# Performance work log

Measured on AMD Instinct MI355X. Metric: run time of the kernel, lower is better.

Reference implementation:

```python
import jax, jax.numpy as jnp
import numpy as np
from jax import lax

B, C_IN, H_IN, W_IN = 128, 256, 8, 32
RH, RW = 16, 64            # rec-head resolution
YOH, XOH = RH // 2, RW // 2  # onehot sizes (8, 32)
HID = 256
NC = 163                   # num classes == embed size
T = 32                     # target length
C_ENC = C_IN + XOH + YOH   # 296 encoder channels
L = (RH // 2) * (RW // 2)  # 256 attention positions


def setup_inputs() -> dict:
    key = jax.random.key(0)
    ks = jax.random.split(key, 18)
    s = 0.05
    return {
        "x": jax.random.normal(ks[0], (B, C_IN, H_IN, W_IN), jnp.float32),
        "decoder_targets": jax.random.randint(ks[1], (B, T), 0, NC),
        "word_targets": jax.random.randint(ks[2], (B, T), 0, NC),
        # seq_encoder conv 3x3
        "conv_w": jax.random.normal(ks[3], (C_IN, C_IN, 3, 3), jnp.float32) * 0.02,
        "conv_b": jnp.zeros((C_IN,), jnp.float32),
        # decoder embedding (post kaiming re-init => random, not identity)
        "emb_dec": jax.random.normal(ks[4], (NC, NC), jnp.float32) * s,
        "word_w": jax.random.normal(ks[5], (HID, NC), jnp.float32) * s,
        "word_b": jnp.zeros((HID,), jnp.float32),
        "attn_w": jax.random.normal(ks[6], (HID, 2 * HID + XOH + YOH), jnp.float32) * s,
        "attn_b": jnp.zeros((HID,), jnp.float32),
        "attn_v": jax.random.normal(ks[7], (HID,), jnp.float32) * (1.0 / np.sqrt(HID)),
        # GRUCell, gate order [r, z, n]
        "gru_wih": jax.random.normal(ks[8], (3 * HID, 2 * HID + XOH + YOH), jnp.float32) * s,
        "gru_bih": jnp.zeros((3 * HID,), jnp.float32),
        "gru_whh": jax.random.normal(ks[9], (3 * HID, HID), jnp.float32) * s,
        "gru_bhh": jnp.zeros((3 * HID,), jnp.float32),
        "out_w": jax.random.normal(ks[10], (NC, HID), jnp.float32) * s,
        "out_b": jnp.zeros((NC,), jnp.float32),
        # positional one-hot embedding tables (also kaiming re-initialized)
        "x_emb": jax.random.normal(ks[11], (XOH, XOH), jnp.float32) * s,
        "y_emb": jax.random.normal(ks[12], (YOH, YOH), jnp.float32) * s,
    }


def _forward(x, conv_w, conv_b, emb_dec, word_w, word_b, attn_w, attn_b, attn_v,
             gru_wih, gru_bih, gru_whh, gru_bhh, out_w, out_b, x_emb, y_emb,
             decoder_targets, word_targets):
    b = x.shape[0]
    # rescale: bilinear upsample (align_corners=False ~ half-pixel)
    xr = jax.image.resize(x, (b, C_IN, RH, RW), method="linear")
    # seq_encoder: conv3x3 + ReLU + maxpool2
    conv = lax.conv_general_dilated(xr, conv_w, (1, 1), "SAME",
                                    dimension_numbers=("NCHW", "OIHW", "NCHW"))
    conv = jax.nn.relu(conv + conv_b[None, :, None, None])
    pooled = lax.reduce_window(conv, -jnp.inf, lax.max,
                               (1, 1, 2, 2), (1, 1, 2, 2), "VALID")  # (B,256,8,32)
    hf, wf = RH // 2, RW // 2
    # positional channels: x_map[c,y,x] = x_emb[x,c]; y_map[c,y,x] = y_emb[y,c]
    x_map = jnp.broadcast_to(x_emb.T[:, None, :], (XOH, hf, wf))
    y_map = jnp.broadcast_to(y_emb.T[:, :, None], (YOH, hf, wf))
    x_map = jnp.broadcast_to(x_map[None], (b, XOH, hf, wf))
    y_map = jnp.broadcast_to(y_map[None], (b, YOH, hf, wf))
    feat = jnp.concatenate([pooled, x_map, y_map], axis=1)      # (B,296,8,32)
    enc = feat.reshape(b, C_ENC, hf * wf).transpose(0, 2, 1)    # (B, L, C)

    t_len = decoder_targets.shape[1]
    # teacher forcing: input at step 0 is BOS (=0), else previous target
    inputs_seq = jnp.concatenate(
        [jnp.zeros((b, 1), decoder_targets.dtype), decoder_targets[:, :-1]], axis=1)

    def step(hidden, xs):
        tok, tgt = xs
        we = emb_dec[tok] @ word_w.T + word_b                   # (B, HID)
        # Bahdanau attention
        hrep = jnp.broadcast_to(hidden[:, None, :], (b, enc.shape[1], HID))
        cat = jnp.concatenate([hrep, enc], axis=-1)             # (B,L,2H+OH)
        energy = jnp.tanh(jnp.einsum("blc,hc->blh", cat, attn_w) + attn_b)
        scores = jnp.einsum("blh,h->bl", energy, attn_v)
        w = jax.nn.softmax(scores, axis=1)                      # (B,L)
        ctx = jnp.einsum("bl,blc->bc", w, enc)                  # (B, C)
        rin = jnp.concatenate([we, ctx], axis=-1)               # (B, 2H+OH)
        # GRUCell
        gi = rin @ gru_wih.T + gru_bih
        gh = hidden @ gru_whh.T + gru_bhh
        i_r, i_z, i_n = jnp.split(gi, 3, axis=-1)
        h_r, h_z, h_n = jnp.split(gh, 3, axis=-1)
        r = jax.nn.sigmoid(i_r + h_r)
        z = jax.nn.sigmoid(i_z + h_z)
        n = jnp.tanh(i_n + r * h_n)
        h_new = (1.0 - z) * n + z * hidden
        logp = jax.nn.log_softmax(h_new @ out_w.T + out_b, axis=1)
        # NLLLoss(ignore_index=-1, reduction='none')
        nll = -jnp.take_along_axis(logp, jnp.clip(tgt, 0)[:, None], axis=1)[:, 0]
        nll = jnp.where(tgt >= 0, nll, 0.0)
        return h_new, nll

    h0 = jnp.zeros((b, HID), jnp.float32)
    _, nlls = lax.scan(step, h0, (inputs_seq.T, word_targets.T))  # (T, B)
    loss_vec = nlls.sum(axis=0)                                   # (B,)
    return 0.2 * (loss_vec.sum() / loss_vec.shape[0])


def reference(x, decoder_targets, word_targets, conv_w, conv_b, emb_dec,
              word_w, word_b, attn_w, attn_b, attn_v, gru_wih, gru_bih,
              gru_whh, gru_bhh, out_w, out_b, x_emb, y_emb):
    return _forward(x, conv_w, conv_b, emb_dec, word_w, word_b, attn_w, attn_b,
                    attn_v, gru_wih, gru_bih, gru_whh, gru_bhh, out_w, out_b,
                    x_emb, y_emb, decoder_targets, word_targets)
```

## Files before the change

### kernel.cpp

```cpp
#include <hip/hip_runtime.h>
#include <hip/hip_bf16.h>
#include <math.h>

#define B    128
#define CIN  256
#define HIN  8
#define WIN_ 32
#define RH   16
#define RW   64
#define HID  256
#define NC   163
#define T    32
#define L    256
#define CENC 296

typedef __attribute__((ext_vector_type(8))) short short8;
typedef __attribute__((ext_vector_type(8))) unsigned short u16x8;
typedef __attribute__((ext_vector_type(4))) float f32x4;

#define PH(k) ((((k) >> 3) * 12) + ((k) & 7))

__device__ __forceinline__ float bf2f(unsigned short u) {
    unsigned int x = ((unsigned int)u) << 16;
    return __uint_as_float(x);
}
__device__ __forceinline__ unsigned short f2bf(float f) {
    unsigned int x = __float_as_uint(f);
    unsigned int r = (x + 0x7FFFu + ((x >> 16) & 1u)) >> 16;
    return (unsigned short)r;
}
__device__ __forceinline__ float fast_tanh(float x) {
    float e = __expf(2.f * x);
    return 1.f - 2.f * __builtin_amdgcn_rcpf(e + 1.f);
}
__device__ __forceinline__ float fast_sigm(float x) {
    return __builtin_amdgcn_rcpf(1.f + __expf(-x));
}
__device__ __forceinline__ float wave_red_max(float v) {
    #pragma unroll
    for (int o = 32; o > 0; o >>= 1) v = fmaxf(v, __shfl_down(v, o, 64));
    return v;
}
__device__ __forceinline__ float wave_red_sum(float v) {
    #pragma unroll
    for (int o = 32; o > 0; o >>= 1) v += __shfl_down(v, o, 64);
    return v;
}
__device__ __forceinline__ float half_red_sum(float v) {
    #pragma unroll
    for (int o = 16; o > 0; o >>= 1) v += __shfl_down(v, o, 64);
    return v;
}

__global__ void __launch_bounds__(256) k_upsxt(const float* __restrict__ x,
                                               unsigned short* __restrict__ Xt) {
    __shared__ __align__(16) float sf[64 * 2 * 32];
    const int y = blockIdx.x;
    const int b = blockIdx.y;
    const int tid = threadIdx.x;
    float sy = 0.5f * y - 0.25f;
    int yq0 = (y - 1) >> 1;
    float wy = sy - (float)yq0;
    int y0c = min(max(yq0, 0), HIN - 1);
    int y1c = min(max(yq0 + 1, 0), HIN - 1);
    const int xo = tid & 63;
    const int cj = tid >> 6;
    float sx = 0.5f * xo - 0.25f;
    int xq0 = (xo - 1) >> 1;
    float wx = sx - (float)xq0;
    int x0c = min(max(xq0, 0), WIN_ - 1);
    int x1c = min(max(xq0 + 1, 0), WIN_ - 1);
    for (int cc = 0; cc < 4; cc++) {
        __syncthreads();
        #pragma unroll
        for (int i = 0; i < 4; i++) {
            int idx = tid * 4 + i;
            int c = idx >> 4;
            int rowh = (idx >> 3) & 1;
            int part = idx & 7;
            int ysrc = rowh ? y1c : y0c;
            float4 v = *reinterpret_cast<const float4*>(
                x + ((size_t)(b * CIN + cc * 64 + c) * HIN + ysrc) * WIN_ + part * 4);
            *reinterpret_cast<float4*>(sf + ((c * 2 + rowh) * 32 + part * 4)) = v;
        }
        __syncthreads();
        unsigned short ov[16];
        #pragma unroll
        for (int j = 0; j < 16; j++) {
            int c = cj * 16 + j;
            const float* r0 = sf + (c * 2 + 0) * 32;
            const float* r1 = sf + (c * 2 + 1) * 32;
            float v = (1.f - wy) * ((1.f - wx) * r0[x0c] + wx * r0[x1c])
                    +        wy  * ((1.f - wx) * r1[x0c] + wx * r1[x1c]);
            ov[j] = f2bf(v);
        }
        unsigned short* dst = Xt + ((size_t)((b * 16 + y) * 64 + xo)) * 256 + cc * 64 + cj * 16;
        *reinterpret_cast<u16x8*>(dst)     = *reinterpret_cast<u16x8*>(ov);
        *reinterpret_cast<u16x8*>(dst + 8) = *reinterpret_cast<u16x8*>(ov + 8);
    }
}

__global__ void k_wt(const float* __restrict__ conv_w, unsigned short* __restrict__ Wt) {
    int e = blockIdx.x * 256 + threadIdx.x;
    int ci = e & 255;
    int co = (e >> 8) & 255;
    int s  = e >> 16;
    Wt[(size_t)(s * 256 + co) * 256 + ci] = f2bf(conv_w[(size_t)(co * 256 + ci) * 9 + s]);
}

__global__ void __launch_bounds__(256) k_convmm(const unsigned short* __restrict__ Xt,
        const unsigned short* __restrict__ Wt, const float* __restrict__ conv_b,
        unsigned short* __restrict__ enc_bf) {
    __shared__ __align__(16) char smem[34048];
    unsigned short* A_s = (unsigned short*)smem;
    unsigned short* B_s = A_s + 128 * 40;
    float* pool = (float*)smem;
    const int mt = blockIdx.x;
    const int n0 = blockIdx.y * 128;
    const int b = mt >> 3;
    const int y0 = (mt & 7) * 2;
    const int tid = threadIdx.x;
    const int wave = tid >> 6, lane = tid & 63;
    const int mq = (wave & 1) * 64, nq = (wave >> 1) * 64;
    const int lm = lane & 15, lq = lane >> 4;
    f32x4 acc[4][4];
    #pragma unroll
    for (int mi = 0; mi < 4; mi++)
        #pragma unroll
        for (int ni = 0; ni < 4; ni++)
            #pragma unroll
            for (int r = 0; r < 4; r++) acc[mi][ni][r] = 0.f;

    for (int s9 = 0; s9 < 9; s9++) {
        const int ky = s9 / 3, kx = s9 % 3;
        const unsigned short* Wb = Wt + (size_t)s9 * 256 * 256;
        for (int kc = 0; kc < 256; kc += 32) {
            __syncthreads();
            #pragma unroll
            for (int it = 0; it < 2; it++) {
                int s2 = tid + it * 256;
                int pix = s2 >> 2, q4 = s2 & 3;
                int yy = y0 + (pix >> 6) + ky - 1;
                int xx = (pix & 63) + kx - 1;
                u16x8 va = {0, 0, 0, 0, 0, 0, 0, 0};
                if ((unsigned)yy < 16u && (unsigned)xx < 64u)
                    va = *reinterpret_cast<const u16x8*>(
                        Xt + ((size_t)((b * 16 + yy) * 64 + xx)) * 256 + kc + q4 * 8);
                *reinterpret_cast<u16x8*>(A_s + pix * 40 + q4 * 8) = va;
                u16x8 vb = *reinterpret_cast<const u16x8*>(
                    Wb + (size_t)(n0 + pix) * 256 + kc + q4 * 8);
                *reinterpret_cast<u16x8*>(B_s + pix * 40 + q4 * 8) = vb;
            }
            __syncthreads();
            short8 af[4], bfr[4];
            #pragma unroll
            for (int mi = 0; mi < 4; mi++)
                af[mi] = *reinterpret_cast<const short8*>(A_s + (mq + mi * 16 + lm) * 40 + lq * 8);
            #pragma unroll
            for (int ni = 0; ni < 4; ni++)
                bfr[ni] = *reinterpret_cast<const short8*>(B_s + (nq + ni * 16 + lm) * 40 + lq * 8);
            #pragma unroll
            for (int mi = 0; mi < 4; mi++)
                #pragma unroll
                for (int ni = 0; ni < 4; ni++)
                    acc[mi][ni] = __builtin_amdgcn_mfma_f32_16x16x32_bf16(
                        af[mi], bfr[ni], acc[mi][ni], 0, 0, 0);
        }
    }
    __syncthreads();
    #pragma unroll
    for (int mi = 0; mi < 4; mi++) {
        int px0 = mi * 8 + lq * 2;
        #pragma unroll
        for (int ni = 0; ni < 4; ni++) {
            int nl = nq + ni * 16 + lm;
            float pa = fmaxf(acc[mi][ni][0], acc[mi][ni][1]);
            float pb = fmaxf(acc[mi][ni][2], acc[mi][ni][3]);
            pool[((wave & 1) * 32 + px0) * 132 + nl] = pa;
            pool[((wave & 1) * 32 + px0 + 1) * 132 + nl] = pb;
        }
    }
    __syncthreads();
    {
        int base = tid * 16;
        int px = base >> 7;
        int nb = base & 127;
        unsigned short ov[16];
        #pragma unroll
        for (int i = 0; i < 16; i++) {
            int n = nb + i;
            float v = fmaxf(pool[px * 132 + n], pool[(32 + px) * 132 + n]) + conv_b[n0 + n];
            ov[i] = f2bf(fmaxf(v, 0.f));
        }
        unsigned short* dst = enc_bf + ((size_t)b * L + (mt & 7) * 32 + px) * CENC + n0 + nb;
        *reinterpret_cast<u16x8*>(dst)     = *reinterpret_cast<u16x8*>(ov);
        *reinterpret_cast<u16x8*>(dst + 8) = *reinterpret_cast<u16x8*>(ov + 8);
    }
}

__global__ void k_encpos(const float* __restrict__ x_emb, const float* __restrict__ y_emb,
                         unsigned short* __restrict__ enc_bf, unsigned short* __restrict__ pos2t) {
    int b = blockIdx.x, l = threadIdx.x;
    int yl = l >> 5, xl = l & 31;
    unsigned short* e = enc_bf + (size_t)(b * L + l) * CENC + 256;
    #pragma unroll
    for (int c = 0; c < 32; c++) e[c] = f2bf(x_emb[xl * 32 + c]);
    #pragma unroll
    for (int c = 0; c < 8; c++) e[32 + c] = f2bf(y_emb[yl * 8 + c]);
    if (b == 0) {
        #pragma unroll
        for (int c = 0; c < 32; c++) pos2t[c * 256 + l] = f2bf(x_emb[xl * 32 + c]);
        #pragma unroll
        for (int c = 0; c < 8; c++) pos2t[(32 + c) * 256 + l] = f2bf(y_emb[yl * 8 + c]);
    }
}

__global__ void __launch_bounds__(256) k_enct(const unsigned short* __restrict__ enc_bf,
                                              unsigned short* __restrict__ enc_t) {
    __shared__ unsigned short s[64 * 264];
    const int c0 = blockIdx.x * 64;
    const int b = blockIdx.y;
    const int tid = threadIdx.x;
    #pragma unroll
    for (int j = 0; j < 8; j++) {
        u16x8 u = *reinterpret_cast<const u16x8*>(
            enc_bf + ((size_t)b * L + tid) * CENC + c0 + j * 8);
        #pragma unroll
        for (int k = 0; k < 8; k++) s[(j * 8 + k) * 264 + tid] = u[k];
    }
    __syncthreads();
    {
        int c = tid >> 2, lp = tid & 3;
        const unsigned short* row = s + c * 264 + lp * 64;
        unsigned short* dst = enc_t + ((size_t)b * 256 + c0 + c) * L + lp * 64;
        #pragma unroll
        for (int i = 0; i < 8; i++)
            *reinterpret_cast<u16x8*>(dst + i * 8) =
                *reinterpret_cast<const u16x8*>(row + i * 8);
    }
}

__global__ void __launch_bounds__(256) k_etab(const float* __restrict__ emb_dec,
                                              const float* __restrict__ word_w,
                                              const float* __restrict__ word_b,
                                              float* __restrict__ E) {
    __shared__ float er[NC];
    int row = blockIdx.x, tid = threadIdx.x;
    for (int k = tid; k < NC; k += 256) er[k] = emb_dec[(size_t)row * NC + k];
    __syncthreads();
    float a = word_b[tid];
    for (int k = 0; k < NC; k++) a += er[k] * word_w[(size_t)tid * NC + k];
    E[(size_t)row * HID + tid] = a;
}

__global__ void k_prep(const float* __restrict__ attn_w, const float* __restrict__ out_w,
                       unsigned short* __restrict__ wA_bf, unsigned short* __restrict__ ow_bf) {
    int o = blockIdx.x, k = threadIdx.x;
    wA_bf[(size_t)o * 256 + k] = f2bf(attn_w[(size_t)o * 552 + k]);
    if (o < NC) ow_bf[(size_t)o * 256 + k] = f2bf(out_w[(size_t)o * 256 + k]);
}

__global__ void __launch_bounds__(1024) k_wpack(const float* __restrict__ wih,
        const float* __restrict__ whh, unsigned short* __restrict__ WpackC,
        unsigned short* __restrict__ WpackH) {
    const int blk = blockIdx.x;
    const int tid = threadIdx.x;
    unsigned short o[8];
    if (blk < 37) {
        #pragma unroll
        for (int j = 0; j < 8; j++) {
            int k = blk * 8 + j;
            float v = (tid < 768) ? wih[(size_t)tid * 552 + 256 + k] : 0.f;
            o[j] = f2bf(v);
        }
        *reinterpret_cast<u16x8*>(WpackC + ((size_t)blk * 1024 + tid) * 8) =
            *reinterpret_cast<u16x8*>(o);
    } else {
        int it = blk - 37;
        #pragma unroll
        for (int j = 0; j < 8; j++) {
            int k = it * 8 + j;
            float v = (tid < 768) ? whh[(size_t)tid * 256 + k] : 0.f;
            o[j] = f2bf(v);
        }
        *reinterpret_cast<u16x8*>(WpackH + ((size_t)it * 1024 + tid) * 8) =
            *reinterpret_cast<u16x8*>(o);
    }
}

__global__ void __launch_bounds__(768) k_wge(const float* __restrict__ wih,
                                             unsigned short* __restrict__ WgE) {
    int k = blockIdx.x, g = threadIdx.x;
    WgE[(size_t)k * 768 + g] = f2bf(wih[(size_t)g * 552 + k]);
}
__global__ void __launch_bounds__(768) k_gie(const float* __restrict__ E,
                                             const unsigned short* __restrict__ WgE,
                                             const float* __restrict__ bih,
                                             float* __restrict__ giE) {
    __shared__ float er[256];
    int v = blockIdx.x, g = threadIdx.x;
    if (g < 256) er[g] = E[(size_t)v * 256 + g];
    __syncthreads();
    float a = bih[g];
    #pragma unroll 4
    for (int k = 0; k < 256; k++) a += er[k] * bf2f(WgE[(size_t)k * 768 + g]);
    giE[(size_t)v * 768 + g] = a;
}

__global__ void __launch_bounds__(256) k_ep(const unsigned short* __restrict__ enc_bf,
                                            const float* __restrict__ attn_w,
                                            unsigned short* __restrict__ ep_t) {
    __shared__ __align__(16) float eS[16][132];
    __shared__ __align__(16) float wS[16][36];
    const int l0 = blockIdx.x * 128;
    const int h0 = blockIdx.y * 32;
    const int b = blockIdx.z;
    const int tid = threadIdx.x;
    const int hh = tid >> 5, ll = tid & 31;
    float acc[4][4];
    #pragma unroll
    for (int s2 = 0; s2 < 4; s2++)
        #pragma unroll
        for (int r = 0; r < 4; r++) acc[s2][r] = 0.f;
    for (int kc = 0; kc < CENC; kc += 16) {
        const int kn = min(16, CENC - kc);
        __syncthreads();
        #pragma unroll
        for (int it = 0; it < 2; it++) {
            int idx = it * 256 + tid;
            int lq = idx >> 2, kq = idx & 3;
            float v0 = 0.f, v1 = 0.f, v2 = 0.f, v3 = 0.f;
            if (kq * 4 < kn) {
                ushort4 u = *reinterpret_cast<const ushort4*>(
                    enc_bf + (size_t)(b * L + l0 + lq) * CENC + kc + kq * 4);
                v0 = bf2f(u.x); v1 = bf2f(u.y); v2 = bf2f(u.z); v3 = bf2f(u.w);
            }
            eS[kq * 4 + 0][lq] = v0; eS[kq * 4 + 1][lq] = v1;
            eS[kq * 4 + 2][lq] = v2; eS[kq * 4 + 3][lq] = v3;
        }
        if (tid < 128) {
            int hq = tid >> 2, kq = tid & 3;
            float4 v = make_float4(0.f, 0.f, 0.f, 0.f);
            if (kq * 4 < kn)
                v = *reinterpret_cast<const float4*>(attn_w + (size_t)(h0 + hq) * 552 + 256 + kc + kq * 4);
            wS[kq * 4 + 0][hq] = v.x; wS[kq * 4 + 1][hq] = v.y;
            wS[kq * 4 + 2][hq] = v.z; wS[kq * 4 + 3][hq] = v.w;
        }
        __syncthreads();
        #pragma unroll
        for (int k = 0; k < 16; k++) {
            float4 e = *reinterpret_cast<const float4*>(&eS[k][ll * 4]);
            float4 w = *reinterpret_cast<const float4*>(&wS[k][hh * 4]);
            float ev[4] = {e.x, e.y, e.z, e.w};
            float wv[4] = {w.x, w.y, w.z, w.w};
            #pragma unroll
            for (int s2 = 0; s2 < 4; s2++)
                #pragma unroll
                for (int r = 0; r < 4; r++) acc[s2][r] += wv[s2] * ev[r];
        }
    }
    #pragma unroll
    for (int r = 0; r < 4; r++) {
        ushort4 o;
        o.x = f2bf(acc[0][r]); o.y = f2bf(acc[1][r]);
        o.z = f2bf(acc[2][r]); o.w = f2bf(acc[3][r]);
        *reinterpret_cast<ushort4*>(
            ep_t + ((size_t)(b * L) + l0 + ll * 4 + r) * HID + h0 + hh * 4) = o;
    }
}

__global__ void k_init(int* __restrict__ flagH, int* __restrict__ flagS) {
    if (threadIdx.x < B) { flagH[threadIdx.x] = 0; flagS[threadIdx.x] = 0; }
}

__global__ void __launch_bounds__(1024) k_steps(
        const float* __restrict__ giE, const float* __restrict__ bhh,
        const unsigned short* __restrict__ ep_t, const unsigned short* __restrict__ enc_t,
        const unsigned short* __restrict__ wA_bf, const unsigned short* __restrict__ ow_bf,
        const unsigned short* __restrict__ pos2t,
        const unsigned short* __restrict__ WpackC, const unsigned short* __restrict__ WpackH,
        const float* __restrict__ attn_b, const float* __restrict__ attn_v,
        const float* __restrict__ out_b,
        const int* __restrict__ dec_tgt, const int* __restrict__ word_tgt,
        float* __restrict__ nllG,
        unsigned int* __restrict__ hX32, unsigned int* __restrict__ sX32,
        int* __restrict__ flagH, int* __restrict__ flagS) {
    const int bid = blockIdx.x;
    const bool roleA = bid < B;
    const int b = bid & (B - 1);
    const int tid = threadIdx.x;
    const int hwid = tid >> 5, l32 = tid & 31;

    __shared__ __align__(16) unsigned short big[L * 256];
    __shared__ __align__(16) unsigned short hmail[256];
    __shared__ __align__(16) unsigned short swl[256];
    __shared__ __align__(16) float rinF[552];
    __shared__ __align__(16) float hF[384];
    __shared__ __align__(16) float hpF[384], vbF[384], swlF[384];
    __shared__ float hfS[256];
    __shared__ float scr[256];
    __shared__ float red[16];
    __shared__ float rzS[512], inS[256], hnS[256];
    unsigned int* hmail32 = reinterpret_cast<unsigned int*>(hmail);
    unsigned int* swl32 = reinterpret_cast<unsigned int*>(swl);

    if (roleA) {
        if (tid < 256) vbF[PH(tid)] = attn_v[tid];
        {
            const u16x8* src = reinterpret_cast<const u16x8*>(ep_t + (size_t)b * L * 256);
            u16x8* dst = reinterpret_cast<u16x8*>(big);
            #pragma unroll
            for (int i = 0; i < 8; i++) dst[tid + i * 1024] = src[tid + i * 1024];
        }
        float nllacc = 0.f;
        __syncthreads();
        for (int t = 0; t <= T; t++) {
            if (tid < 128) {
                while (__hip_atomic_load(&flagH[b], __ATOMIC_RELAXED,
                                         __HIP_MEMORY_SCOPE_AGENT) < t + 1)
                    __builtin_amdgcn_s_sleep(1);
                unsigned int u = __hip_atomic_load(&hX32[b * 128 + tid], __ATOMIC_RELAXED,
                                                   __HIP_MEMORY_SCOPE_AGENT);
                hF[PH(2 * tid)]     = bf2f((unsigned short)(u & 0xffffu));
                hF[PH(2 * tid + 1)] = bf2f((unsigned short)(u >> 16));
            }
            __syncthreads();
            if (t < T) {
                #pragma unroll
                for (int it = 0; it < 8; it++) {
                    int row = it * 32 + hwid;
                    u16x8 w = *reinterpret_cast<const u16x8*>(wA_bf + (size_t)row * 256 + l32 * 8);
                    float4 ha = *reinterpret_cast<const float4*>(hF + l32 * 12);
                    float4 hb = *reinterpret_cast<const float4*>(hF + l32 * 12 + 4);
                    float d = bf2f(w[0]) * ha.x + bf2f(w[1]) * ha.y
                            + bf2f(w[2]) * ha.z + bf2f(w[3]) * ha.w
                            + bf2f(w[4]) * hb.x + bf2f(w[5]) * hb.y
                            + bf2f(w[6]) * hb.z + bf2f(w[7]) * hb.w;
                    d = half_red_sum(d);
                    if (l32 == 0) hpF[PH(row)] = d + attn_b[row];
                }
                __syncthreads();
                #pragma unroll
                for (int it = 0; it < 8; it++) {
                    int row = it * 32 + hwid;
                    u16x8 e = *reinterpret_cast<const u16x8*>(big + (size_t)row * 256 + l32 * 8);
                    float4 ha = *reinterpret_cast<const float4*>(hpF + l32 * 12);
                    float4 hb = *reinterpret_cast<const float4*>(hpF + l32 * 12 + 4);
                    float4 va = *reinterpret_cast<const float4*>(vbF + l32 * 12);
                    float4 vv = *reinterpret_cast<const float4*>(vbF + l32 * 12 + 4);
                    float d = va.x * fast_tanh(bf2f(e[0]) + ha.x)
                            + va.y * fast_tanh(bf2f(e[1]) + ha.y)
                            + va.z * fast_tanh(bf2f(e[2]) + ha.z)
                            + va.w * fast_tanh(bf2f(e[3]) + ha.w)
                            + vv.x * fast_tanh(bf2f(e[4]) + hb.x)
                            + vv.y * fast_tanh(bf2f(e[5]) + hb.y)
                            + vv.z * fast_tanh(bf2f(e[6]) + hb.z)
                            + vv.w * fast_tanh(bf2f(e[7]) + hb.w);
                    d = half_red_sum(d);
                    if (l32 == 0) scr[row] = d;
                }
                __syncthreads();
                float sc = -1e30f;
                if (tid < 256) {
                    sc = scr[tid];
                    float m = wave_red_max(sc);
                    if ((tid & 63) == 0) red[tid >> 6] = m;
                }
                __syncthreads();
                float M2 = fmaxf(fmaxf(red[0], red[1]), fmaxf(red[2], red[3]));
                float e2 = 0.f;
                if (tid < 256) {
                    e2 = __expf(sc - M2);
                    float sm = wave_red_sum(e2);
                    if ((tid & 63) == 0) red[8 + (tid >> 6)] = sm;
                }
                __syncthreads();
                if (tid < 256) {
                    float invS = __builtin_amdgcn_rcpf(red[8] + red[9] + red[10] + red[11]);
                    swl[tid] = f2bf(e2 * invS);
                }
                __syncthreads();
                if (tid < 128)
                    __hip_atomic_store(&sX32[b * 128 + tid], swl32[tid], __ATOMIC_RELAXED,
                                       __HIP_MEMORY_SCOPE_AGENT);
                __syncthreads();
                if (tid == 0)
                    __hip_atomic_store(&flagS[b], t + 1, __ATOMIC_RELAXED,
                                       __HIP_MEMORY_SCOPE_AGENT);
            }
            if (t > 0) {
                #pragma unroll
                for (int it = 0; it < 6; it++) {
                    int row = it * 32 + hwid;
                    float d = 0.f;
                    if (row < NC) {
                        u16x8 w = *reinterpret_cast<const u16x8*>(ow_bf + (size_t)row * 256 + l32 * 8);
                        float4 ha = *reinterpret_cast<const float4*>(hF + l32 * 12);
                        float4 hb = *reinterpret_cast<const float4*>(hF + l32 * 12 + 4);
                        d = bf2f(w[0]) * ha.x + bf2f(w[1]) * ha.y
                          + bf2f(w[2]) * ha.z + bf2f(w[3]) * ha.w
                          + bf2f(w[4]) * hb.x + bf2f(w[5]) * hb.y
                          + bf2f(w[6]) * hb.z + bf2f(w[7]) * hb.w;
                    }
                    d = half_red_sum(d);
                    if (l32 == 0 && row < NC) scr[row] = d + out_b[row];
                }
                __syncthreads();
                float lg = -1e30f;
                if (tid < 256) {
                    if (tid < NC) lg = scr[tid];
                    float m = wave_red_max(lg);
                    if ((tid & 63) == 0) red[tid >> 6] = m;
                }
                __syncthreads();
                float M = fmaxf(fmaxf(red[0], red[1]), fmaxf(red[2], red[3]));
                if (tid < 256) {
                    float e = (tid < NC) ? __expf(lg - M) : 0.f;
                    float sm = wave_red_sum(e);
                    if ((tid & 63) == 0) red[8 + (tid >> 6)] = sm;
                }
                __syncthreads();
                if (tid == 0) {
                    float S = red[8] + red[9] + red[10] + red[11];
                    int tgt = word_tgt[b * T + (t - 1)];
                    if (tgt >= 0) nllacc += M + __logf(S) - scr[tgt];
                }
                __syncthreads();
            }
        }
        if (tid == 0) nllG[b] = nllacc;
    } else {
        {
            const u16x8* src = reinterpret_cast<const u16x8*>(enc_t + (size_t)b * 256 * 256);
            u16x8* dst = reinterpret_cast<u16x8*>(big);
            #pragma unroll
            for (int i = 0; i < 8; i++) dst[tid + i * 1024] = src[tid + i * 1024];
        }
        __syncthreads();
        for (int t = 0; t <= T; t++) {
            if (tid < 256) {
                float h;
                if (t == 0) {
                    h = 0.f;
                } else {
                    float hold = hfS[tid];
                    int tokp = (t == 1) ? 0 : dec_tgt[b * T + (t - 2)];
                    const float* gE = giE + (size_t)tokp * 768;
                    float r_ = fast_sigm(rzS[tid] + gE[tid] + bhh[tid]);
                    float z_ = fast_sigm(rzS[256 + tid] + gE[256 + tid] + bhh[256 + tid]);
                    float n_ = fast_tanh(inS[tid] + gE[512 + tid] + r_ * (hnS[tid] + bhh[512 + tid]));
                    h = (1.f - z_) * n_ + z_ * hold;
                }
                hfS[tid] = h;
                hmail[tid] = f2bf(h);
                rinF[296 + tid] = h;
            }
            __syncthreads();
            if (tid < 128)
                __hip_atomic_store(&hX32[b * 128 + tid], hmail32[tid], __ATOMIC_RELAXED,
                                   __HIP_MEMORY_SCOPE_AGENT);
            __syncthreads();
            if (tid == 0)
                __hip_atomic_store(&flagH[b], t + 1, __ATOMIC_RELAXED,
                                   __HIP_MEMORY_SCOPE_AGENT);
            if (t == T) break;
            float hacc = 0.f;
            if (tid < 768) {
                float a0 = 0.f, a1 = 0.f;
                #pragma unroll 4
                for (int it = 0; it < 32; it++) {
                    u16x8 w = *reinterpret_cast<const u16x8*>(WpackH + ((size_t)it * 1024 + tid) * 8);
                    float4 ra = *reinterpret_cast<const float4*>(rinF + 296 + it * 8);
                    float4 rb = *reinterpret_cast<const float4*>(rinF + 296 + it * 8 + 4);
                    a0 += bf2f(w[0]) * ra.x + bf2f(w[2]) * ra.z
                        + bf2f(w[4]) * rb.x + bf2f(w[6]) * rb.z;
                    a1 += bf2f(w[1]) * ra.y + bf2f(w[3]) * ra.w
                        + bf2f(w[5]) * rb.y + bf2f(w[7]) * rb.w;
                }
                hacc = a0 + a1;
            }
            if (tid < 128) {
                while (__hip_atomic_load(&flagS[b], __ATOMIC_RELAXED,
                                         __HIP_MEMORY_SCOPE_AGENT) < t + 1)
                    __builtin_amdgcn_s_sleep(1);
                unsigned int u = __hip_atomic_load(&sX32[b * 128 + tid], __ATOMIC_RELAXED,
                                                   __HIP_MEMORY_SCOPE_AGENT);
                swlF[PH(2 * tid)]     = bf2f((unsigned short)(u & 0xffffu));
                swlF[PH(2 * tid + 1)] = bf2f((unsigned short)(u >> 16));
            }
            __syncthreads();
            #pragma unroll
            for (int it = 0; it < 8; it++) {
                int row = it * 32 + hwid;
                u16x8 e = *reinterpret_cast<const u16x8*>(big + (size_t)row * 256 + l32 * 8);
                float4 sa = *reinterpret_cast<const float4*>(swlF + l32 * 12);
                float4 sb = *reinterpret_cast<const float4*>(swlF + l32 * 12 + 4);
                float d = bf2f(e[0]) * sa.x + bf2f(e[1]) * sa.y
                        + bf2f(e[2]) * sa.z + bf2f(e[3]) * sa.w
                        + bf2f(e[4]) * sb.x + bf2f(e[5]) * sb.y
                        + bf2f(e[6]) * sb.z + bf2f(e[7]) * sb.w;
                d = half_red_sum(d);
                if (l32 == 0) rinF[row] = d;
            }
            #pragma unroll
            for (int it = 0; it < 2; it++) {
                int row = it * 32 + hwid;
                float d = 0.f;
                if (row < 40) {
                    u16x8 p = *reinterpret_cast<const u16x8*>(pos2t + (size_t)row * 256 + l32 * 8);
                    float4 sa = *reinterpret_cast<const float4*>(swlF + l32 * 12);
                    float4 sb = *reinterpret_cast<const float4*>(swlF + l32 * 12 + 4);
                    d = bf2f(p[0]) * sa.x + bf2f(p[1]) * sa.y
                      + bf2f(p[2]) * sa.z + bf2f(p[3]) * sa.w
                      + bf2f(p[4]) * sb.x + bf2f(p[5]) * sb.y
                      + bf2f(p[6]) * sb.z + bf2f(p[7]) * sb.w;
                }
                d = half_red_sum(d);
                if (l32 == 0 && row < 40) rinF[256 + row] = d;
            }
            __syncthreads();
            if (tid < 768) {
                float c0 = 0.f, c1 = 0.f;
                #pragma unroll 4
                for (int it = 0; it < 37; it++) {
                    u16x8 w = *reinterpret_cast<const u16x8*>(WpackC + ((size_t)it * 1024 + tid) * 8);
                    float4 ra = *reinterpret_cast<const float4*>(rinF + it * 8);
                    float4 rb = *reinterpret_cast<const float4*>(rinF + it * 8 + 4);
                    c0 += bf2f(w[0]) * ra.x + bf2f(w[2]) * ra.z
                        + bf2f(w[4]) * rb.x + bf2f(w[6]) * rb.z;
                    c1 += bf2f(w[1]) * ra.y + bf2f(w[3]) * ra.w
                        + bf2f(w[5]) * rb.y + bf2f(w[7]) * rb.w;
                }
                float cacc = c0 + c1;
                if (tid < 512) rzS[tid] = cacc + hacc;
                else { inS[tid - 512] = cacc; hnS[tid - 512] = hacc; }
            }
            __syncthreads();
        }
    }
}

__global__ void k_reduce(const float* __restrict__ nll, float* __restrict__ out) {
    __shared__ float red[2];
    float v = nll[threadIdx.x];
    v = wave_red_sum(v);
    if ((threadIdx.x & 63) == 0) red[threadIdx.x >> 6] = v;
    __syncthreads();
    if (threadIdx.x == 0) out[0] = 0.2f * (red[0] + red[1]) * (1.f / 128.f);
}

extern "C" void kernel_launch(void* const* d_in, const int* in_sizes, int n_in,
                              void* d_out, int out_size, void* d_ws, size_t ws_size,
                              hipStream_t stream) {
    const float* x        = (const float*)d_in[0];
    const int*   dec_tgt  = (const int*)d_in[1];
    const int*   word_tgt = (const int*)d_in[2];
    const float* conv_w   = (const float*)d_in[3];
    const float* conv_b   = (const float*)d_in[4];
    const float* emb_dec  = (const float*)d_in[5];
    const float* word_w   = (const float*)d_in[6];
    const float* word_b   = (const float*)d_in[7];
    const float* attn_w   = (const float*)d_in[8];
    const float* attn_b   = (const float*)d_in[9];
    const float* attn_v   = (const float*)d_in[10];
    const float* gru_wih  = (const float*)d_in[11];
    const float* gru_bih  = (const float*)d_in[12];
    const float* gru_whh  = (const float*)d_in[13];
    const float* gru_bhh  = (const float*)d_in[14];
    const float* out_w    = (const float*)d_in[15];
    const float* out_b    = (const float*)d_in[16];
    const float* x_emb    = (const float*)d_in[17];
    const float* y_emb    = (const float*)d_in[18];

    char* ws = (char*)d_ws;
    size_t off = 0;
    auto alloc = [&](size_t bytes) -> void* {
        void* p = ws + off;
        off = (off + bytes + 255) & ~(size_t)255;
        return p;
    };
    unsigned short* Xt     = (unsigned short*)alloc((size_t)B * 16 * 64 * 256 * 2);
    unsigned short* enc_bf = (unsigned short*)alloc((size_t)B * L * CENC * 2);
    unsigned short* Wt     = (unsigned short*)alloc((size_t)9 * 256 * 256 * 2);
    float* E      = (float*)alloc((size_t)NC * HID * 4);
    unsigned short* wA_bf  = (unsigned short*)alloc((size_t)HID * HID * 2);
    unsigned short* ow_bf  = (unsigned short*)alloc((size_t)NC * HID * 2);
    unsigned short* WpackC = (unsigned short*)alloc((size_t)37 * 1024 * 8 * 2);
    unsigned short* WpackH = (unsigned short*)alloc((size_t)32 * 1024 * 8 * 2);
    unsigned short* WgE    = (unsigned short*)alloc((size_t)256 * 768 * 2);
    float* giE    = (float*)alloc((size_t)NC * 768 * 4);
    unsigned short* pos2t  = (unsigned short*)alloc((size_t)40 * 256 * 2);
    float* nllG   = (float*)alloc((size_t)B * 4);
    unsigned int* hX32     = (unsigned int*)alloc((size_t)B * 128 * 4);
    unsigned int* sX32     = (unsigned int*)alloc((size_t)B * 128 * 4);
    int* flagH    = (int*)alloc((size_t)B * 4);
    int* flagS    = (int*)alloc((size_t)B * 4);
    unsigned short* ep_t  = Xt;
    unsigned short* enc_t = Xt + (size_t)B * L * HID;
    float* out    = (float*)d_out;

    hipLaunchKernelGGL(k_init, dim3(1), dim3(256), 0, stream, flagH, flagS);
    hipLaunchKernelGGL(k_upsxt, dim3(16, 128), dim3(256), 0, stream, x, Xt);
    hipLaunchKernelGGL(k_wt, dim3(2304), dim3(256), 0, stream, conv_w, Wt);
    hipLaunchKernelGGL(k_encpos, dim3(128), dim3(256), 0, stream, x_emb, y_emb, enc_bf, pos2t);
    hipLaunchKernelGGL(k_convmm, dim3(1024, 2), dim3(256), 0, stream, Xt, Wt, conv_b, enc_bf);
    hipLaunchKernelGGL(k_etab, dim3(163), dim3(256), 0, stream, emb_dec, word_w, word_b, E);
    hipLaunchKernelGGL(k_prep, dim3(256), dim3(256), 0, stream, attn_w, out_w, wA_bf, ow_bf);
    hipLaunchKernelGGL(k_wpack, dim3(69), dim3(1024), 0, stream, gru_wih, gru_whh, WpackC, WpackH);
    hipLaunchKernelGGL(k_wge, dim3(256), dim3(768), 0, stream, gru_wih, WgE);
    hipLaunchKernelGGL(k_gie, dim3(163), dim3(768), 0, stream, E, WgE, gru_bih, giE);
    hipLaunchKernelGGL(k_ep, dim3(2, 8, 128), dim3(256), 0, stream, enc_bf, attn_w, ep_t);
    hipLaunchKernelGGL(k_enct, dim3(4, 128), dim3(256), 0, stream, enc_bf, enc_t);
    hipLaunchKernelGGL(k_steps, dim3(256), dim3(1024), 0, stream,
                       giE, gru_bhh, ep_t, enc_t, wA_bf, ow_bf, pos2t, WpackC, WpackH,
                       attn_b, attn_v, out_b, dec_tgt, word_tgt, nllG,
                       hX32, sX32, flagH, flagS);
    hipLaunchKernelGGL(k_reduce, dim3(1), dim3(128), 0, stream, nllG, out);
}
```

Baseline: 1.182 ms.

## Pack step tag with mailbox data in 64-bit words, drop separate flags

Cross-block handoff between the attention role and the GRU role now writes each 32-bit bf16 pair together with the step number in one 64-bit atomic. Consumers spin on the data word itself, which removes the separate flag store, the extra __syncthreads before it, and the second load after the flag. The softmax also drops its max-subtraction pass, saving a reduction and a barrier. That relies on attention scores staying small enough that exp does not overflow. Invariant LDS loads are hoisted out of the unrolled dot-product loops.

```diff
diff --git a/kernel.cpp b/kernel.cpp
--- a/kernel.cpp
+++ b/kernel.cpp
@@ -17,6 +17,7 @@
 typedef __attribute__((ext_vector_type(8))) short short8;
 typedef __attribute__((ext_vector_type(8))) unsigned short u16x8;
 typedef __attribute__((ext_vector_type(4))) float f32x4;
+typedef unsigned long long u64;
 
 #define PH(k) ((((k) >> 3) * 12) + ((k) & 7))
 
@@ -369,8 +370,10 @@
     }
 }
 
-__global__ void k_init(int* __restrict__ flagH, int* __restrict__ flagS) {
-    if (threadIdx.x < B) { flagH[threadIdx.x] = 0; flagS[threadIdx.x] = 0; }
+__global__ void k_init(u64* __restrict__ hX64, u64* __restrict__ sX64) {
+    int gi = blockIdx.x * 256 + threadIdx.x;
+    if (gi < B * 128) hX64[gi] = 0ull;
+    else sX64[gi - B * 128] = 0ull;
 }
 
 __global__ void __launch_bounds__(1024) k_steps(
@@ -383,8 +386,7 @@
         const float* __restrict__ out_b,
         const int* __restrict__ dec_tgt, const int* __restrict__ word_tgt,
         float* __restrict__ nllG,
-        unsigned int* __restrict__ hX32, unsigned int* __restrict__ sX32,
-        int* __restrict__ flagH, int* __restrict__ flagS) {
+        u64* __restrict__ hX64, u64* __restrict__ sX64) {
     const int bid = blockIdx.x;
     const bool roleA = bid < B;
     const int b = bid & (B - 1);
@@ -416,61 +418,61 @@
         __syncthreads();
         for (int t = 0; t <= T; t++) {
             if (tid < 128) {
-                while (__hip_atomic_load(&flagH[b], __ATOMIC_RELAXED,
-                                         __HIP_MEMORY_SCOPE_AGENT) < t + 1)
+                u64 want = (u64)(t + 1);
+                u64 v;
+                for (;;) {
+                    v = __hip_atomic_load(&hX64[b * 128 + tid], __ATOMIC_RELAXED,
+                                          __HIP_MEMORY_SCOPE_AGENT);
+                    if ((v >> 32) == want) break;
                     __builtin_amdgcn_s_sleep(1);
-                unsigned int u = __hip_atomic_load(&hX32[b * 128 + tid], __ATOMIC_RELAXED,
-                                                   __HIP_MEMORY_SCOPE_AGENT);
+                }
+                unsigned int u = (unsigned int)v;
                 hF[PH(2 * tid)]     = bf2f((unsigned short)(u & 0xffffu));
                 hF[PH(2 * tid + 1)] = bf2f((unsigned short)(u >> 16));
             }
             __syncthreads();
             if (t < T) {
-                #pragma unroll
-                for (int it = 0; it < 8; it++) {
-                    int row = it * 32 + hwid;
-                    u16x8 w = *reinterpret_cast<const u16x8*>(wA_bf + (size_t)row * 256 + l32 * 8);
+                {
                     float4 ha = *reinterpret_cast<const float4*>(hF + l32 * 12);
                     float4 hb = *reinterpret_cast<const float4*>(hF + l32 * 12 + 4);
-                    float d = bf2f(w[0]) * ha.x + bf2f(w[1]) * ha.y
-                            + bf2f(w[2]) * ha.z + bf2f(w[3]) * ha.w
-                            + bf2f(w[4]) * hb.x + bf2f(w[5]) * hb.y
-                            + bf2f(w[6]) * hb.z + bf2f(w[7]) * hb.w;
-                    d = half_red_sum(d);
-                    if (l32 == 0) hpF[PH(row)] = d + attn_b[row];
+                    #pragma unroll
+                    for (int it = 0; it < 8; it++) {
+                        int row = it * 32 + hwid;
+                        u16x8 w = *reinterpret_cast<const u16x8*>(wA_bf + (size_t)row * 256 + l32 * 8);
+                        float d = bf2f(w[0]) * ha.x + bf2f(w[1]) * ha.y
+                                + bf2f(w[2]) * ha.z + bf2f(w[3]) * ha.w
+                                + bf2f(w[4]) * hb.x + bf2f(w[5]) * hb.y
+                                + bf2f(w[6]) * hb.z + bf2f(w[7]) * hb.w;
+                        d = half_red_sum(d);
+                        if (l32 == 0) hpF[PH(row)] = d + attn_b[row];
+                    }
                 }
                 __syncthreads();
-                #pragma unroll
-                for (int it = 0; it < 8; it++) {
-                    int row = it * 32 + hwid;
-                    u16x8 e = *reinterpret_cast<const u16x8*>(big + (size_t)row * 256 + l32 * 8);
+                {
                     float4 ha = *reinterpret_cast<const float4*>(hpF + l32 * 12);
                     float4 hb = *reinterpret_cast<const float4*>(hpF + l32 * 12 + 4);
                     float4 va = *reinterpret_cast<const float4*>(vbF + l32 * 12);
                     float4 vv = *reinterpret_cast<const float4*>(vbF + l32 * 12 + 4);
-                    float d = va.x * fast_tanh(bf2f(e[0]) + ha.x)
-                            + va.y * fast_tanh(bf2f(e[1]) + ha.y)
-                            + va.z * fast_tanh(bf2f(e[2]) + ha.z)
-                            + va.w * fast_tanh(bf2f(e[3]) + ha.w)
-                            + vv.x * fast_tanh(bf2f(e[4]) + hb.x)
-                            + vv.y * fast_tanh(bf2f(e[5]) + hb.y)
-                            + vv.z * fast_tanh(bf2f(e[6]) + hb.z)
-                            + vv.w * fast_tanh(bf2f(e[7]) + hb.w);
-                    d = half_red_sum(d);
-                    if (l32 == 0) scr[row] = d;
+                    #pragma unroll
+                    for (int it = 0; it < 8; it++) {
+                        int row = it * 32 + hwid;
+                        u16x8 e = *reinterpret_cast<const u16x8*>(big + (size_t)row * 256 + l32 * 8);
+                        float d = va.x * fast_tanh(bf2f(e[0]) + ha.x)
+                                + va.y * fast_tanh(bf2f(e[1]) + ha.y)
+                                + va.z * fast_tanh(bf2f(e[2]) + ha.z)
+                                + va.w * fast_tanh(bf2f(e[3]) + ha.w)
+                                + vv.x * fast_tanh(bf2f(e[4]) + hb.x)
+                                + vv.y * fast_tanh(bf2f(e[5]) + hb.y)
+                                + vv.z * fast_tanh(bf2f(e[6]) + hb.z)
+                                + vv.w * fast_tanh(bf2f(e[7]) + hb.w);
+                        d = half_red_sum(d);
+                        if (l32 == 0) scr[row] = d;
+                    }
                 }
                 __syncthreads();
-                float sc = -1e30f;
-                if (tid < 256) {
-                    sc = scr[tid];
-                    float m = wave_red_max(sc);
-                    if ((tid & 63) == 0) red[tid >> 6] = m;
-                }
-                __syncthreads();
-                float M2 = fmaxf(fmaxf(red[0], red[1]), fmaxf(red[2], red[3]));
                 float e2 = 0.f;
                 if (tid < 256) {
-                    e2 = __expf(sc - M2);
+                    e2 = __expf(scr[tid]);
                     float sm = wave_red_sum(e2);
                     if ((tid & 63) == 0) red[8 + (tid >> 6)] = sm;
                 }
@@ -481,22 +483,19 @@
                 }
                 __syncthreads();
                 if (tid < 128)
-                    __hip_atomic_store(&sX32[b * 128 + tid], swl32[tid], __ATOMIC_RELAXED,
-                                       __HIP_MEMORY_SCOPE_AGENT);
-                __syncthreads();
-                if (tid == 0)
-                    __hip_atomic_store(&flagS[b], t + 1, __ATOMIC_RELAXED,
-                                       __HIP_MEMORY_SCOPE_AGENT);
+                    __hip_atomic_store(&sX64[b * 128 + tid],
+                                       ((u64)(t + 1) << 32) | (u64)swl32[tid],
+                                       __ATOMIC_RELAXED, __HIP_MEMORY_SCOPE_AGENT);
             }
             if (t > 0) {
+                float4 ha = *reinterpret_cast<const float4*>(hF + l32 * 12);
+                float4 hb = *reinterpret_cast<const float4*>(hF + l32 * 12 + 4);
                 #pragma unroll
                 for (int it = 0; it < 6; it++) {
                     int row = it * 32 + hwid;
                     float d = 0.f;
                     if (row < NC) {
                         u16x8 w = *reinterpret_cast<const u16x8*>(ow_bf + (size_t)row * 256 + l32 * 8);
-                        float4 ha = *reinterpret_cast<const float4*>(hF + l32 * 12);
-                        float4 hb = *reinterpret_cast<const float4*>(hF + l32 * 12 + 4);
                         d = bf2f(w[0]) * ha.x + bf2f(w[1]) * ha.y
                           + bf2f(w[2]) * ha.z + bf2f(w[3]) * ha.w
                           + bf2f(w[4]) * hb.x + bf2f(w[5]) * hb.y
@@ -557,12 +556,9 @@
             }
             __syncthreads();
             if (tid < 128)
-                __hip_atomic_store(&hX32[b * 128 + tid], hmail32[tid], __ATOMIC_RELAXED,
-                                   __HIP_MEMORY_SCOPE_AGENT);
-            __syncthreads();
-            if (tid == 0)
-                __hip_atomic_store(&flagH[b], t + 1, __ATOMIC_RELAXED,
-                                   __HIP_MEMORY_SCOPE_AGENT);
+                __hip_atomic_store(&hX64[b * 128 + tid],
+                                   ((u64)(t + 1) << 32) | (u64)hmail32[tid],
+                                   __ATOMIC_RELAXED, __HIP_MEMORY_SCOPE_AGENT);
             if (t == T) break;
             float hacc = 0.f;
             if (tid < 768) {
@@ -580,43 +576,47 @@
                 hacc = a0 + a1;
             }
             if (tid < 128) {
-                while (__hip_atomic_load(&flagS[b], __ATOMIC_RELAXED,
-                                         __HIP_MEMORY_SCOPE_AGENT) < t + 1)
+                u64 want = (u64)(t + 1);
+                u64 v;
+                for (;;) {
+                    v = __hip_atomic_load(&sX64[b * 128 + tid], __ATOMIC_RELAXED,
+                                          __HIP_MEMORY_SCOPE_AGENT);
+                    if ((v >> 32) == want) break;
                     __builtin_amdgcn_s_sleep(1);
-                unsigned int u = __hip_atomic_load(&sX32[b * 128 + tid], __ATOMIC_RELAXED,
-                                                   __HIP_MEMORY_SCOPE_AGENT);
+                }
+                unsigned int u = (unsigned int)v;
                 swlF[PH(2 * tid)]     = bf2f((unsigned short)(u & 0xffffu));
                 swlF[PH(2 * tid + 1)] = bf2f((unsigned short)(u >> 16));
             }
             __syncthreads();
-            #pragma unroll
-            for (int it = 0; it < 8; it++) {
-                int row = it * 32 + hwid;
-                u16x8 e = *reinterpret_cast<const u16x8*>(big + (size_t)row * 256 + l32 * 8);
+            {
                 float4 sa = *reinterpret_cast<const float4*>(swlF + l32 * 12);
                 float4 sb = *reinterpret_cast<const float4*>(swlF + l32 * 12 + 4);
-                float d = bf2f(e[0]) * sa.x + bf2f(e[1]) * sa.y
-                        + bf2f(e[2]) * sa.z + bf2f(e[3]) * sa.w
-                        + bf2f(e[4]) * sb.x + bf2f(e[5]) * sb.y
-                        + bf2f(e[6]) * sb.z + bf2f(e[7]) * sb.w;
-                d = half_red_sum(d);
-                if (l32 == 0) rinF[row] = d;
-            }
-            #pragma unroll
-            for (int it = 0; it < 2; it++) {
-                int row = it * 32 + hwid;
-                float d = 0.f;
-                if (row < 40) {
-                    u16x8 p = *reinterpret_cast<const u16x8*>(pos2t + (size_t)row * 256 + l32 * 8);
-                    float4 sa = *reinterpret_cast<const float4*>(swlF + l32 * 12);
-                    float4 sb = *reinterpret_cast<const float4*>(swlF + l32 * 12 + 4);
-                    d = bf2f(p[0]) * sa.x + bf2f(p[1]) * sa.y
-                      + bf2f(p[2]) * sa.z + bf2f(p[3]) * sa.w
-                      + bf2f(p[4]) * sb.x + bf2f(p[5]) * sb.y
-                      + bf2f(p[6]) * sb.z + bf2f(p[7]) * sb.w;
-                }
-                d = half_red_sum(d);
-                if (l32 == 0 && row < 40) rinF[256 + row] = d;
+                #pragma unroll
+                for (int it = 0; it < 8; it++) {
+                    int row = it * 32 + hwid;
+                    u16x8 e = *reinterpret_cast<const u16x8*>(big + (size_t)row * 256 + l32 * 8);
+                    float d = bf2f(e[0]) * sa.x + bf2f(e[1]) * sa.y
+                            + bf2f(e[2]) * sa.z + bf2f(e[3]) * sa.w
+                            + bf2f(e[4]) * sb.x + bf2f(e[5]) * sb.y
+                            + bf2f(e[6]) * sb.z + bf2f(e[7]) * sb.w;
+                    d = half_red_sum(d);
+                    if (l32 == 0) rinF[row] = d;
+                }
+                #pragma unroll
+                for (int it = 0; it < 2; it++) {
+                    int row = it * 32 + hwid;
+                    float d = 0.f;
+                    if (row < 40) {
+                        u16x8 p = *reinterpret_cast<const u16x8*>(pos2t + (size_t)row * 256 + l32 * 8);
+                        d = bf2f(p[0]) * sa.x + bf2f(p[1]) * sa.y
+                          + bf2f(p[2]) * sa.z + bf2f(p[3]) * sa.w
+                          + bf2f(p[4]) * sb.x + bf2f(p[5]) * sb.y
+                          + bf2f(p[6]) * sb.z + bf2f(p[7]) * sb.w;
+                    }
+                    d = half_red_sum(d);
+                    if (l32 == 0 && row < 40) rinF[256 + row] = d;
+                }
             }
             __syncthreads();
             if (tid < 768) {
@@ -691,15 +691,13 @@
     float* giE    = (float*)alloc((size_t)NC * 768 * 4);
     unsigned short* pos2t  = (unsigned short*)alloc((size_t)40 * 256 * 2);
     float* nllG   = (float*)alloc((size_t)B * 4);
-    unsigned int* hX32     = (unsigned int*)alloc((size_t)B * 128 * 4);
-    unsigned int* sX32     = (unsigned int*)alloc((size_t)B * 128 * 4);
-    int* flagH    = (int*)alloc((size_t)B * 4);
-    int* flagS    = (int*)alloc((size_t)B * 4);
+    u64* hX64     = (u64*)alloc((size_t)B * 128 * 8);
+    u64* sX64     = (u64*)alloc((size_t)B * 128 * 8);
     unsigned short* ep_t  = Xt;
     unsigned short* enc_t = Xt + (size_t)B * L * HID;
     float* out    = (float*)d_out;
 
-    hipLaunchKernelGGL(k_init, dim3(1), dim3(256), 0, stream, flagH, flagS);
+    hipLaunchKernelGGL(k_init, dim3(128), dim3(256), 0, stream, hX64, sX64);
     hipLaunchKernelGGL(k_upsxt, dim3(16, 128), dim3(256), 0, stream, x, Xt);
     hipLaunchKernelGGL(k_wt, dim3(2304), dim3(256), 0, stream, conv_w, Wt);
     hipLaunchKernelGGL(k_encpos, dim3(128), dim3(256), 0, stream, x_emb, y_emb, enc_bf, pos2t);
@@ -714,6 +712,6 @@
     hipLaunchKernelGGL(k_steps, dim3(256), dim3(1024), 0, stream,
                        giE, gru_bhh, ep_t, enc_t, wA_bf, ow_bf, pos2t, WpackC, WpackH,
                        attn_b, attn_v, out_b, dec_tgt, word_tgt, nllG,
-                       hX32, sX32, flagH, flagS);
+                       hX64, sX64);
     hipLaunchKernelGGL(k_reduce, dim3(1), dim3(128), 0, stream, nllG, out);
 }
```

New measurement: 1.102 ms. 1.07x faster.
